# Performance work log

Hardware: AMD Instinct MI355X
Metric: run time of the kernel (lower is better)

## Reference

```python
import jax, jax.numpy as jnp
import numpy as np


def conv2d(x, w, groups=1, pad=0):
    # x: [N,C,H,W], w: [O, C//groups, kh, kw]
    return jax.lax.conv_general_dilated(
        x, w, window_strides=(1, 1), padding=[(pad, pad), (pad, pad)],
        dimension_numbers=("NCHW", "OIHW", "NCHW"), feature_group_count=groups)


def l2norm(x, eps=1e-12):
    # torch F.normalize over last dim: x / max(||x||_2, eps)
    n = jnp.sqrt(jnp.sum(x * x, axis=-1, keepdims=True))
    return x / jnp.maximum(n, eps)


def setup_inputs() -> dict:
    key = jax.random.key(0)
    dim, heads, b, H, W = 48, 8, 2, 256, 256
    ks = jax.random.split(key, 20)
    rn = lambda k, shp, s: (jax.random.normal(k, shp, dtype=jnp.float32) * s)
    return {
        "x1": rn(ks[0], (b, dim, H, W), 1.0),
        "x2": rn(ks[1], (b, dim, H, W), 1.0),
        "t1": jnp.ones((heads, 1, 1), jnp.float32),
        "t2": jnp.ones((heads, 1, 1), jnp.float32),
        "qkv1_w": rn(ks[2], (dim * 3, dim, 1, 1), 0.05),
        "qkv1_dw": rn(ks[3], (dim * 3, 1, 3, 3), 0.05),
        "qkv2_w": rn(ks[4], (dim * 3, dim, 1, 1), 0.05),
        "qkv2_dw": rn(ks[5], (dim * 3, 1, 3, 3), 0.05),
        "mid1_w": rn(ks[6], (dim, dim, 1, 1), 0.05),
        "mid2_w": rn(ks[7], (dim, dim, 1, 1), 0.05),
        "pE_w": rn(ks[8], (dim * 8, dim * 2, 1, 1), 0.05),
        "pE_dw": rn(ks[9], (dim * 8, 1, 3, 3), 0.05),
        "pE1_w": rn(ks[10], (dim * 4, dim, 1, 1), 0.05),
        "pE1_dw": rn(ks[11], (dim * 4, 1, 3, 3), 0.05),
        "pE2_w": rn(ks[12], (dim * 4, dim, 1, 1), 0.05),
        "pE2_dw": rn(ks[13], (dim * 4, 1, 3, 3), 0.05),
        "po1_w": rn(ks[14], (dim * 2, dim * 4, 1, 1), 0.05),
        "po2_w": rn(ks[15], (dim * 2, dim * 4, 1, 1), 0.05),
    }


def reference(x1, x2, t1, t2, qkv1_w, qkv1_dw, qkv2_w, qkv2_dw,
              mid1_w, mid2_w, pE_w, pE_dw, pE1_w, pE1_dw,
              pE2_w, pE2_dw, po1_w, po2_w):
    b, c, h, w = x1.shape
    heads = t1.shape[0]
    ch = c // heads  # channels per head

    def to_heads(t):  # [b, c, h, w] -> [b, heads, ch, h*w]
        return t.reshape(b, heads, ch, h * w)

    qkv1 = conv2d(conv2d(x1, qkv1_w), qkv1_dw, groups=3 * c, pad=1)
    q1, k1, v1 = jnp.split(qkv1, 3, axis=1)
    qkv2 = conv2d(conv2d(x2, qkv2_w), qkv2_dw, groups=3 * c, pad=1)
    q2, k2, v2 = jnp.split(qkv2, 3, axis=1)

    q1, k1, v1 = to_heads(q1), to_heads(k1), to_heads(v1)
    q2, k2, v2 = to_heads(q2), to_heads(k2), to_heads(v2)
    q1, k1 = l2norm(q1), l2norm(k1)
    q2, k2 = l2norm(q2), l2norm(k2)

    # channel cross-attention: [b, heads, ch, ch]
    attn1 = jnp.einsum("bhcn,bhdn->bhcd", q2, k1) * t1
    attn2 = jnp.einsum("bhcn,bhdn->bhcd", q1, k2) * t2
    out1 = jnp.einsum("bhcd,bhdn->bhcn", jax.nn.softmax(attn1, axis=-1), v1)
    out2 = jnp.einsum("bhcd,bhdn->bhcn", jax.nn.softmax(attn2, axis=-1), v2)
    out1 = out1.reshape(b, c, h, w)
    out2 = out2.reshape(b, c, h, w)

    x1 = x1 + conv2d(out1, mid1_w)
    x2 = x2 + conv2d(out2, mid2_w)
    out = jnp.concatenate([x1, x2], axis=1)  # [b, 2c, h, w]

    g = conv2d(conv2d(out, pE_w), pE_dw, groups=8 * c, pad=1)  # [b, 8c, h, w]
    g1, g2 = jnp.split(g, 2, axis=1)
    x1 = jax.nn.gelu(g1, approximate=False) * conv2d(conv2d(x1, pE1_w), pE1_dw, groups=4 * c, pad=1)
    x2 = jax.nn.gelu(g2, approximate=False) * conv2d(conv2d(x2, pE2_w), pE2_dw, groups=4 * c, pad=1)

    return out + conv2d(x1, po1_w) + conv2d(x2, po2_w)
```

## Files before the change

### kernel.cpp

```cpp
#include <hip/hip_runtime.h>
#include <math.h>

#define HW_ 65536

typedef __attribute__((ext_vector_type(8))) short b16x8;
typedef __attribute__((ext_vector_type(4))) short b16x4;
typedef __attribute__((ext_vector_type(4))) float f32x4;

__device__ __forceinline__ unsigned short f2b(float f) {
    union { float f; unsigned u; } v; v.f = f;
    unsigned r = v.u + 0x7fffu + ((v.u >> 16) & 1u);
    return (unsigned short)(r >> 16);
}
__device__ __forceinline__ float b2f(unsigned short h) {
    union { unsigned u; float f; } v; v.u = ((unsigned)h) << 16; return v.f;
}
__device__ __forceinline__ float gelu_f(float x) {
    float t = 0.7978845608f * fmaf(0.044715f * x, x * x, x);
    float e = __expf(2.f * t);
    float th = 1.f - 2.f / (e + 1.f);
    return 0.5f * x * (1.f + th);
}

__device__ __forceinline__ float wave_reduce_sum(float v) {
    #pragma unroll
    for (int off = 32; off; off >>= 1) v += __shfl_down(v, off, 64);
    return v;
}

__device__ __forceinline__ size_t baddr(long px, int CC, int g) {
    return (((size_t)(px >> 4)) * CC + g) * 128 + ((size_t)(px & 15) << 3);
}

__global__ __launch_bounds__(256) void wprep_k(
    const float* __restrict__ q1w, const float* __restrict__ q2w,
    const float* __restrict__ m1w, const float* __restrict__ m2w,
    const float* __restrict__ pEw, const float* __restrict__ p1w,
    const float* __restrict__ p2w, const float* __restrict__ o1w,
    const float* __restrict__ o2w,
    const float* __restrict__ q1dw, const float* __restrict__ q2dw,
    const float* __restrict__ pEdw, const float* __restrict__ p1dw,
    const float* __restrict__ p2dw,
    unsigned short* __restrict__ wt, float* __restrict__ dwt)
{
    const int idx = blockIdx.x * 256 + threadIdx.x;
    if (idx < 135168) {
        const int base[8] = {0,9216,18432,21504,24576,61440,98304,116736};
        int s = 0;
        #pragma unroll
        for (int i = 1; i < 8; i++) if (idx >= base[i]) s = i;
        const int local = idx - base[s];
        float v = 0.f;
        if (s < 4) {
            const int m = local >> 6, k = local & 63;
            const float* src = (s == 0) ? q1w : (s == 1) ? q2w : (s == 2) ? m1w : m2w;
            if (k < 48) v = src[m * 48 + k];
        } else if (s < 6) {
            const int br = s - 4;
            const int m = local / 96, k = local % 96;
            if (m < 192) {
                v = pEw[(size_t)(br * 192 + m) * 96 + k];
            } else {
                const float* p12 = br ? p2w : p1w;
                const int lo = br * 48, m2 = m - 192;
                if (k >= lo && k < lo + 48) v = p12[m2 * 48 + (k - lo)];
            }
        } else {
            const int m = local / 192, k = local % 192;
            v = ((s == 6) ? o1w : o2w)[m * 192 + k];
        }
        wt[idx] = f2b(v);
    } else if (idx < 135168 + 9504) {
        const int d = idx - 135168;
        const int dbase[5] = {0,1296,2592,6048,7776};
        const int Cs[5] = {144,144,384,192,192};
        int s = 0;
        #pragma unroll
        for (int i = 1; i < 5; i++) if (d >= dbase[i]) s = i;
        const int local = d - dbase[s], C = Cs[s];
        const int t = local / C, c = local % C;
        const float* src = (s == 0) ? q1dw : (s == 1) ? q2dw : (s == 2) ? pEdw
                         : (s == 3) ? p1dw : p2dw;
        dwt[d] = src[c * 9 + t];
    }
}

template<int BM, int KC, int NT, int BSRC, int EPI, bool GRIDSWAP>
__global__ __launch_bounds__(256) void gemm_k(
    const unsigned short* __restrict__ B16,
    const float* __restrict__ Bf32, int Cin,
    const unsigned short* __restrict__ W16,
    unsigned short* __restrict__ out16, int CCo, int Coff,
    float* __restrict__ outf, const unsigned short* __restrict__ res,
    const unsigned short* __restrict__ acc16)
{
    constexpr int MF = BM / 16;
    const int tid = threadIdx.x;
    const int lane = tid & 63, w = tid >> 6;
    const int lm = lane & 15, lk = lane >> 4;
    const int mb = GRIDSWAP ? blockIdx.x : blockIdx.y;
    const int pxblk = GRIDSWAP ? blockIdx.y : blockIdx.x;
    const int m0 = mb * BM;
    const long wavepx = ((long)pxblk * 4 + w) * (NT * 16);
    const long pxb0 = wavepx >> 4;

    f32x4 acc[NT][MF];
    #pragma unroll
    for (int nt = 0; nt < NT; nt++)
        #pragma unroll
        for (int m = 0; m < MF; m++)
            #pragma unroll
            for (int j = 0; j < 4; j++) acc[nt][m][j] = 0.f;

    #pragma unroll
    for (int kc = 0; kc < KC; kc++) {
        b16x8 a[MF];
        #pragma unroll
        for (int m = 0; m < MF; m++)
            a[m] = *(const b16x8*)&W16[(size_t)(m0 + m * 16 + lm) * (KC * 32) + kc * 32 + lk * 8];
        #pragma unroll
        for (int nt = 0; nt < NT; nt++) {
            b16x8 bb;
            if (BSRC == 0) {
                bb = *(const b16x8*)&B16[((pxb0 + nt) * (KC * 4) + (kc * 4 + lk)) * 128 + lm * 8];
            } else {
                const long px = wavepx + nt * 16 + lm;
                const int p = (int)(px & 65535), bat = (int)(px >> 16);
                #pragma unroll
                for (int j = 0; j < 8; j++) {
                    const int c = kc * 32 + lk * 8 + j;
                    float v = (c < Cin) ? Bf32[((size_t)(bat * Cin + c) << 16) + p] : 0.f;
                    bb[j] = (short)f2b(v);
                }
            }
            #pragma unroll
            for (int m = 0; m < MF; m++)
                acc[nt][m] = __builtin_amdgcn_mfma_f32_16x16x32_bf16(a[m], bb, acc[nt][m], 0, 0, 0);
        }
    }

    #pragma unroll
    for (int nt = 0; nt < NT; nt++) {
        const long px = wavepx + nt * 16 + lm;
        #pragma unroll
        for (int m = 0; m < MF; m++) {
            const int mrow = m * 16 + lk * 4;
            if (EPI == 0) {
                b16x4 o;
                #pragma unroll
                for (int j = 0; j < 4; j++) o[j] = (short)f2b(acc[nt][m][j]);
                const int ch = Coff + m0 + mrow;
                *(b16x4*)&out16[((pxb0 + nt) * CCo + (ch >> 3)) * 128 + lm * 8 + (ch & 7)] = o;
            } else if (EPI == 1) {
                const int p = (int)(px & 65535), bat = (int)(px >> 16);
                b16x4 r4 = *(const b16x4*)&res[((pxb0 + nt) * 12 + (mrow >> 3)) * 128 + lm * 8 + (mrow & 7)];
                #pragma unroll
                for (int j = 0; j < 4; j++)
                    outf[((size_t)(bat * 96 + mrow + j) << 16) + p]
                        = acc[nt][m][j] + b2f((unsigned short)r4[j]);
            } else if (EPI == 2) {
                const int p = (int)(px & 65535), bat = (int)(px >> 16);
                #pragma unroll
                for (int j = 0; j < 4; j++) {
                    const size_t adr = ((size_t)(bat * 96 + mrow + j) << 16) + p;
                    outf[adr] += acc[nt][m][j];
                }
            } else {
                const int p = (int)(px & 65535), bat = (int)(px >> 16);
                const size_t boffi = ((pxb0 + nt) * 12 + (mrow >> 3)) * 128 + lm * 8 + (mrow & 7);
                b16x4 r4 = *(const b16x4*)&res[boffi];
                b16x4 a4 = *(const b16x4*)&acc16[boffi];
                #pragma unroll
                for (int j = 0; j < 4; j++)
                    outf[((size_t)(bat * 96 + mrow + j) << 16) + p]
                        = acc[nt][m][j] + b2f((unsigned short)r4[j]) + b2f((unsigned short)a4[j]);
            }
        }
    }
}

__device__ __forceinline__ void unpack8(const uint4 u, float f[8]) {
    union { unsigned u; float f; } a;
    a.u = u.x << 16;         f[0] = a.f;
    a.u = u.x & 0xFFFF0000u; f[1] = a.f;
    a.u = u.y << 16;         f[2] = a.f;
    a.u = u.y & 0xFFFF0000u; f[3] = a.f;
    a.u = u.z << 16;         f[4] = a.f;
    a.u = u.z & 0xFFFF0000u; f[5] = a.f;
    a.u = u.w << 16;         f[6] = a.f;
    a.u = u.w & 0xFFFF0000u; f[7] = a.f;
}

__device__ __forceinline__ void dw_row4(
    float acc[4][8], const unsigned short* __restrict__ T,
    size_t cb, long lOff, long rOff, bool lval, bool rval,
    const float* __restrict__ wrow, int wstr)
{
    float w[3][8];
    #pragma unroll
    for (int tx = 0; tx < 3; tx++) {
        const float4 a = *(const float4*)(wrow + (size_t)tx * wstr);
        const float4 b = *(const float4*)(wrow + (size_t)tx * wstr + 4);
        w[tx][0] = a.x; w[tx][1] = a.y; w[tx][2] = a.z; w[tx][3] = a.w;
        w[tx][4] = b.x; w[tx][5] = b.y; w[tx][6] = b.z; w[tx][7] = b.w;
    }
    uint4 u[6];
    if (lval) u[0] = *(const uint4*)&T[cb + lOff];
    else      u[0] = make_uint4(0u, 0u, 0u, 0u);
    #pragma unroll
    for (int c = 0; c < 4; c++) u[c + 1] = *(const uint4*)&T[cb + (size_t)c * 8];
    if (rval) u[5] = *(const uint4*)&T[cb + rOff];
    else      u[5] = make_uint4(0u, 0u, 0u, 0u);

    #pragma unroll
    for (int d = 0; d < 6; d++) {
        float f[8];
        unpack8(u[d], f);
        #pragma unroll
        for (int tx = 0; tx < 3; tx++) {
            const int p = d - tx;
            if (p >= 0 && p < 4)
                #pragma unroll
                for (int j = 0; j < 8; j++)
                    acc[p][j] = fmaf(w[tx][j], f[j], acc[p][j]);
        }
    }
}

__global__ __launch_bounds__(256) void dw144_k(
    const unsigned short* __restrict__ in1, unsigned short* __restrict__ out1,
    const unsigned short* __restrict__ in2, unsigned short* __restrict__ out2,
    const float* __restrict__ dwt)
{
    const int z = blockIdx.z;
    const unsigned short* in = z ? in2 : in1;
    unsigned short* out = z ? out2 : out1;
    const float* wt = dwt + z * 1296;
    const int bx = blockIdx.x;
    const int sb = (bx & 7) * 288 + (bx >> 3);
    const int idx = sb * 256 + threadIdx.x;
    const int pbi = idx / 72;
    const int rem = idx - pbi * 72;
    const int g = rem >> 2, i = rem & 3;
    const long px0 = (long)pbi * 16 + i * 4;
    const int x0 = (int)(px0 & 255);
    const int y = (int)((px0 >> 8) & 255);
    const bool lval = x0 > 0, rval = x0 < 252;
    const int off = (int)(px0 & 15) * 8;
    const size_t cb0 = ((size_t)(px0 >> 4) * 18 + g) * 128 + off;
    const long lOff = (off == 0) ? (120 - 18 * 128) : -8;
    const long rOff = (off == 96) ? (18 * 128 - 96) : 32;
    const long dyStep = 16 * 18 * 128;

    float acc[4][8];
    #pragma unroll
    for (int p = 0; p < 4; p++)
        #pragma unroll
        for (int j = 0; j < 8; j++) acc[p][j] = 0.f;

    #pragma unroll
    for (int dy = -1; dy <= 1; dy++) {
        const int yy = y + dy;
        if ((unsigned)yy >= 256u) continue;
        const size_t cb = cb0 + (size_t)((long)dy * dyStep);
        dw_row4(acc, in, cb, lOff, rOff, lval, rval,
                wt + g * 8 + (size_t)(dy + 1) * 3 * 144, 144);
    }

    #pragma unroll
    for (int p = 0; p < 4; p++) {
        b16x8 o;
        #pragma unroll
        for (int j = 0; j < 8; j++) o[j] = (short)f2b(acc[p][j]);
        *(b16x8*)&out[cb0 + (size_t)p * 8] = o;
    }
}

__global__ __launch_bounds__(256) void dwtail_k(
    const unsigned short* __restrict__ GH, unsigned short* __restrict__ Xg,
    const float* __restrict__ dwtG, const float* __restrict__ dwtH)
{
    const int bx = blockIdx.x;
    const int sb = (bx & 7) * 384 + (bx >> 3);
    const int idx = sb * 256 + threadIdx.x;
    const int pbi = idx / 96;
    const int rem = idx - pbi * 96;
    const int g = rem >> 2, i = rem & 3;
    const long px0 = (long)pbi * 16 + i * 4;
    const int x0 = (int)(px0 & 255);
    const int y = (int)((px0 >> 8) & 255);
    const bool lval = x0 > 0, rval = x0 < 252;
    const int off = (int)(px0 & 15) * 8;
    const size_t cb0 = ((size_t)(px0 >> 4) * 48 + g) * 128 + off;
    const long lOff = (off == 0) ? (120 - 48 * 128) : -8;
    const long rOff = (off == 96) ? (48 * 128 - 96) : 32;
    const long dyStep = 16 * 48 * 128;

    float aG[4][8], aH[4][8];
    #pragma unroll
    for (int p = 0; p < 4; p++)
        #pragma unroll
        for (int j = 0; j < 8; j++) { aG[p][j] = 0.f; aH[p][j] = 0.f; }

    #pragma unroll
    for (int dy = -1; dy <= 1; dy++) {
        const int yy = y + dy;
        if ((unsigned)yy >= 256u) continue;
        const size_t cb = cb0 + (size_t)((long)dy * dyStep);
        dw_row4(aG, GH, cb, lOff, rOff, lval, rval,
                dwtG + g * 8 + (size_t)(dy + 1) * 3 * 384, 384);
        dw_row4(aH, GH, cb + 3072, lOff, rOff, lval, rval,
                dwtH + g * 8 + (size_t)(dy + 1) * 3 * 192, 192);
    }

    const size_t ob = ((size_t)(px0 >> 4) * 24 + g) * 128 + off;
    #pragma unroll
    for (int p = 0; p < 4; p++) {
        b16x8 o;
        #pragma unroll
        for (int j = 0; j < 8; j++)
            o[j] = (short)f2b(gelu_f(aG[p][j]) * aH[p][j]);
        *(b16x8*)&Xg[ob + (size_t)p * 8] = o;
    }
}

__global__ __launch_bounds__(256) void attnA_k(
    const unsigned short* __restrict__ Q1, const unsigned short* __restrict__ Q2,
    float* __restrict__ part)
{
    const int tid = threadIdx.x;
    const int chunk = blockIdx.x, bh = blockIdx.y, a = blockIdx.z;
    const int b = bh >> 3, h = bh & 7;
    const unsigned* Qq = (const unsigned*)(a ? Q1 : Q2);
    const unsigned* Qk = (const unsigned*)(a ? Q2 : Q1);
    const int u0 = h * 3;
    const int cq = u0 >> 2, o = u0 & 3;
    const int ck = (24 + u0) >> 2;

    float dot[36], nq[6], nk[6];
    #pragma unroll
    for (int i = 0; i < 36; i++) dot[i] = 0.f;
    #pragma unroll
    for (int i = 0; i < 6; i++) { nq[i] = 0.f; nk[i] = 0.f; }

    #pragma unroll 1
    for (int r = 0; r < 8; r++) {
        const long px = (long)b * 65536 + chunk * 2048 + r * 256 + tid;
        const size_t rowu = ((size_t)(px >> 4)) * 18 * 64 + ((px & 15) << 2);
        const uint4 qa = *(const uint4*)&Qq[rowu + (size_t)cq * 64];
        const uint4 qb = *(const uint4*)&Qq[rowu + (size_t)(cq + 1) * 64];
        const uint4 ka = *(const uint4*)&Qk[rowu + (size_t)ck * 64];
        const uint4 kb = *(const uint4*)&Qk[rowu + (size_t)(ck + 1) * 64];
        unsigned uq[3], uk[3];
        if (o == 0)      { uq[0]=qa.x; uq[1]=qa.y; uq[2]=qa.z; uk[0]=ka.x; uk[1]=ka.y; uk[2]=ka.z; }
        else if (o == 1) { uq[0]=qa.y; uq[1]=qa.z; uq[2]=qa.w; uk[0]=ka.y; uk[1]=ka.z; uk[2]=ka.w; }
        else if (o == 2) { uq[0]=qa.z; uq[1]=qa.w; uq[2]=qb.x; uk[0]=ka.z; uk[1]=ka.w; uk[2]=kb.x; }
        else             { uq[0]=qa.w; uq[1]=qb.x; uq[2]=qb.y; uk[0]=ka.w; uk[1]=kb.x; uk[2]=kb.y; }
        float q[6], k[6];
        #pragma unroll
        for (int i = 0; i < 3; i++) {
            union { unsigned u; float f; } lo, hi;
            lo.u = uq[i] << 16; hi.u = uq[i] & 0xFFFF0000u;
            q[2 * i] = lo.f; q[2 * i + 1] = hi.f;
            lo.u = uk[i] << 16; hi.u = uk[i] & 0xFFFF0000u;
            k[2 * i] = lo.f; k[2 * i + 1] = hi.f;
        }
        #pragma unroll
        for (int c = 0; c < 6; c++) nq[c] = fmaf(q[c], q[c], nq[c]);
        #pragma unroll
        for (int d = 0; d < 6; d++) nk[d] = fmaf(k[d], k[d], nk[d]);
        #pragma unroll
        for (int c = 0; c < 6; c++)
            #pragma unroll
            for (int d = 0; d < 6; d++) dot[c * 6 + d] = fmaf(q[c], k[d], dot[c * 6 + d]);
    }

    __shared__ float red[4][48];
    const int lane = tid & 63, wid = tid >> 6;
    #pragma unroll
    for (int i = 0; i < 48; i++) {
        float v = (i < 36) ? dot[i] : (i < 42 ? nq[i - 36] : nk[i - 42]);
        v = wave_reduce_sum(v);
        if (!lane) red[wid][i] = v;
    }
    __syncthreads();
    if (tid < 48)
        part[((size_t)((a * 16 + bh) * 32 + chunk)) * 48 + tid]
            = red[0][tid] + red[1][tid] + red[2][tid] + red[3][tid];
}

__global__ void attnB_k(const float* __restrict__ part,
                        const float* __restrict__ t1, const float* __restrict__ t2,
                        float* __restrict__ att)
{
    const int abh = blockIdx.x, tid = threadIdx.x;
    const int a = abh >> 4, b = (abh >> 3) & 1, h = abh & 7;
    __shared__ float s[48];
    if (tid < 48) {
        float v = 0.f;
        for (int ch = 0; ch < 32; ch++) v += part[((size_t)abh * 32 + ch) * 48 + tid];
        s[tid] = v;
    }
    __syncthreads();
    if (tid < 6) {
        const int c = tid;
        const float tv = a ? t2[h] : t1[h];
        const float qn = fmaxf(sqrtf(s[36 + c]), 1e-12f);
        float raw[6];
        #pragma unroll
        for (int d = 0; d < 6; d++)
            raw[d] = tv * s[c * 6 + d] / (qn * fmaxf(sqrtf(s[42 + d]), 1e-12f));
        float m = raw[0];
        #pragma unroll
        for (int d = 1; d < 6; d++) m = fmaxf(m, raw[d]);
        float e[6], sum = 0.f;
        #pragma unroll
        for (int d = 0; d < 6; d++) { e[d] = expf(raw[d] - m); sum += e[d]; }
        const float inv = 1.f / sum;
        #pragma unroll
        for (int d = 0; d < 6; d++)
            att[((size_t)(a * 2 + b) * 8 + h) * 36 + c * 6 + d] = e[d] * inv;
    }
}

__global__ __launch_bounds__(256) void mid_k(
    const unsigned short* __restrict__ Q1, const unsigned short* __restrict__ Q2,
    const float* __restrict__ att,
    const float* __restrict__ x1, const float* __restrict__ x2,
    const unsigned short* __restrict__ Wm, unsigned short* __restrict__ D16p)
{
    const int br = blockIdx.y;
    const unsigned short* Qv = br ? Q2 : Q1;
    const float* x = br ? x2 : x1;
    const unsigned short* W16 = Wm + br * 3072;
    const float* attb = att + br * 576;
    const int boff = br * 48;

    __shared__ float atts[288];
    __shared__ unsigned short S[256][72];
    const int tid = threadIdx.x;
    const long px = (long)blockIdx.x * 256 + tid;
    const int bat = (int)(px >> 16);

    for (int i = tid; i < 288; i += 256) atts[i] = attb[bat * 288 + i];

    float v[48];
    #pragma unroll
    for (int i = 0; i < 6; i++) {
        b16x8 t = *(const b16x8*)&Qv[baddr(px, 18, 12 + i)];
        #pragma unroll
        for (int j = 0; j < 8; j++) v[i * 8 + j] = b2f((unsigned short)t[j]);
    }
    __syncthreads();

    #pragma unroll
    for (int h = 0; h < 8; h++) {
        unsigned short sh[6];
        #pragma unroll
        for (int c = 0; c < 6; c++) {
            float s = 0.f;
            #pragma unroll
            for (int d = 0; d < 6; d++) s = fmaf(atts[h * 36 + c * 6 + d], v[h * 6 + d], s);
            sh[c] = f2b(s);
        }
        #pragma unroll
        for (int i = 0; i < 3; i++) {
            unsigned packed = (unsigned)sh[2 * i] | ((unsigned)sh[2 * i + 1] << 16);
            *(unsigned*)&S[tid][h * 6 + 2 * i] = packed;
        }
    }
    #pragma unroll
    for (int i = 0; i < 8; i++) *(unsigned*)&S[tid][48 + 2 * i] = 0u;
    __syncthreads();

    const int lane = tid & 63, w = tid >> 6;
    const int lm = lane & 15, lk = lane >> 4;
    f32x4 acc[4][3];
    #pragma unroll
    for (int nt = 0; nt < 4; nt++)
        #pragma unroll
        for (int m = 0; m < 3; m++)
            #pragma unroll
            for (int j = 0; j < 4; j++) acc[nt][m][j] = 0.f;

    #pragma unroll
    for (int kc = 0; kc < 2; kc++) {
        b16x8 a[3];
        #pragma unroll
        for (int m = 0; m < 3; m++)
            a[m] = *(const b16x8*)&W16[(size_t)(m * 16 + lm) * 64 + kc * 32 + lk * 8];
        #pragma unroll
        for (int nt = 0; nt < 4; nt++) {
            b16x8 bb = *(const b16x8*)&S[w * 64 + nt * 16 + lm][kc * 32 + lk * 8];
            #pragma unroll
            for (int m = 0; m < 3; m++)
                acc[nt][m] = __builtin_amdgcn_mfma_f32_16x16x32_bf16(a[m], bb, acc[nt][m], 0, 0, 0);
        }
    }

    #pragma unroll
    for (int nt = 0; nt < 4; nt++) {
        const long px2 = (long)blockIdx.x * 256 + w * 64 + nt * 16 + lm;
        const int p2 = (int)(px2 & 65535);
        const long pxb2 = px2 >> 4;
        #pragma unroll
        for (int m = 0; m < 3; m++) {
            const int row = m * 16 + lk * 4;
            b16x4 o;
            #pragma unroll
            for (int j = 0; j < 4; j++) {
                float xv = x[((size_t)(bat * 48 + row + j) << 16) + p2];
                o[j] = (short)f2b(acc[nt][m][j] + xv);
            }
            const int ch = boff + row;
            *(b16x4*)&D16p[(pxb2 * 12 + (ch >> 3)) * 128 + lm * 8 + (ch & 7)] = o;
        }
    }
}

extern "C" void kernel_launch(void* const* d_in, const int* in_sizes, int n_in,
                              void* d_out, int out_size, void* d_ws, size_t ws_size,
                              hipStream_t stream) {
    const float* x1      = (const float*)d_in[0];
    const float* x2      = (const float*)d_in[1];
    const float* t1      = (const float*)d_in[2];
    const float* t2      = (const float*)d_in[3];
    const float* qkv1_w  = (const float*)d_in[4];
    const float* qkv1_dw = (const float*)d_in[5];
    const float* qkv2_w  = (const float*)d_in[6];
    const float* qkv2_dw = (const float*)d_in[7];
    const float* mid1_w  = (const float*)d_in[8];
    const float* mid2_w  = (const float*)d_in[9];
    const float* pE_w    = (const float*)d_in[10];
    const float* pE_dw   = (const float*)d_in[11];
    const float* pE1_w   = (const float*)d_in[12];
    const float* pE1_dw  = (const float*)d_in[13];
    const float* pE2_w   = (const float*)d_in[14];
    const float* pE2_dw  = (const float*)d_in[15];
    const float* po1_w   = (const float*)d_in[16];
    const float* po2_w   = (const float*)d_in[17];
    float* dout = (float*)d_out;
    char* ws = (char*)d_ws;

    unsigned short* D16p  = (unsigned short*)(ws + 0);
    unsigned short* QKVc1 = (unsigned short*)(ws + 25165824);
    unsigned short* QKVc2 = (unsigned short*)(ws + 62914560);
    unsigned short* Q1    = (unsigned short*)(ws + 100663296);
    unsigned short* Q2    = (unsigned short*)(ws + 138412032);
    unsigned short* GH    = (unsigned short*)(ws + 25165824);
    unsigned short* Xg    = (unsigned short*)(ws + 125829120);
    float*          PART  = (float*)(ws + 176160768);
    float*          ATT   = (float*)(ws + 176357376);
    unsigned short* W16   = (unsigned short*)(ws + 176361984);
    float*          DWT   = (float*)(ws + 176632320);
    unsigned short* ACC   = (unsigned short*)(ws + 176670720);

    const dim3 blk(256);

    wprep_k<<<dim3(566), blk, 0, stream>>>(
        qkv1_w, qkv2_w, mid1_w, mid2_w, pE_w, pE1_w, pE2_w, po1_w, po2_w,
        qkv1_dw, qkv2_dw, pE_dw, pE1_dw, pE2_dw, W16, DWT);

    gemm_k<144,2,2,1,0,false><<<dim3(1024,1), blk, 0, stream>>>(
        nullptr, x1, 48, W16, QKVc1, 18, 0, nullptr, nullptr, nullptr);
    gemm_k<144,2,2,1,0,false><<<dim3(1024,1), blk, 0, stream>>>(
        nullptr, x2, 48, W16 + 9216, QKVc2, 18, 0, nullptr, nullptr, nullptr);
    dw144_k<<<dim3(2304,1,2), blk, 0, stream>>>(QKVc1, Q1, QKVc2, Q2, DWT);

    attnA_k<<<dim3(32,16,2), blk, 0, stream>>>(Q1, Q2, PART);
    attnB_k<<<dim3(32), dim3(64), 0, stream>>>(PART, t1, t2, ATT);

    mid_k<<<dim3(512,2), blk, 0, stream>>>(Q1, Q2, ATT, x1, x2, W16 + 18432, D16p);

    for (int br = 0; br < 2; br++) {
        gemm_k<96,3,2,0,0,true><<<dim3(4,1024), blk, 0, stream>>>(
            D16p, nullptr, 0, W16 + 24576 + br * 36864, GH, 48, 0,
            nullptr, nullptr, nullptr);
        dwtail_k<<<dim3(3072), blk, 0, stream>>>(
            GH, Xg, DWT + 2592 + br * 192, DWT + (br ? 7776 : 6048));
        if (br == 0)
            gemm_k<96,6,2,0,0,false><<<dim3(1024,1), blk, 0, stream>>>(
                Xg, nullptr, 0, W16 + 98304, ACC, 12, 0, nullptr, nullptr, nullptr);
        else
            gemm_k<96,6,2,0,3,false><<<dim3(1024,1), blk, 0, stream>>>(
                Xg, nullptr, 0, W16 + 116736, nullptr, 0, 0, dout, D16p, ACC);
    }
}
```

Baseline: 400.9 us.

## Fuse depthwise gelu-gate tail with po projection GEMM via shared memory

The depthwise 3x3 + GELU gating kernel and the following po 1x1 projection GEMM are merged into one kernel. Each 384-thread block computes a 64-pixel tile of the gated activations into LDS, then runs MFMA bf16 matmuls against the po weights and writes either the bf16 partial accumulator or the final fp32 output with residuals. This removes the global round trip of the Xg intermediate and one launch per branch. In exchange the block has lower parallelism for the GEMM, uses LDS per block, and reloads weights from global per block.

```diff
diff --git a/kernel.cpp b/kernel.cpp
--- a/kernel.cpp
+++ b/kernel.cpp
@@ -276,51 +276,105 @@
     }
 }
 
-__global__ __launch_bounds__(256) void dwtail_k(
-    const unsigned short* __restrict__ GH, unsigned short* __restrict__ Xg,
-    const float* __restrict__ dwtG, const float* __restrict__ dwtH)
-{
+template<int EPI>
+__global__ __launch_bounds__(384) void dwpo_k(
+    const unsigned short* __restrict__ GH,
+    const float* __restrict__ dwtG, const float* __restrict__ dwtH,
+    const unsigned short* __restrict__ Wpo,
+    unsigned short* __restrict__ ACC, float* __restrict__ dout,
+    const unsigned short* __restrict__ res,
+    const unsigned short* __restrict__ acc16)
+{
+    __shared__ unsigned short XgS[4 * 24 * 136];
     const int bx = blockIdx.x;
-    const int sb = (bx & 7) * 384 + (bx >> 3);
-    const int idx = sb * 256 + threadIdx.x;
-    const int pbi = idx / 96;
-    const int rem = idx - pbi * 96;
-    const int g = rem >> 2, i = rem & 3;
-    const long px0 = (long)pbi * 16 + i * 4;
-    const int x0 = (int)(px0 & 255);
-    const int y = (int)((px0 >> 8) & 255);
-    const bool lval = x0 > 0, rval = x0 < 252;
-    const int off = (int)(px0 & 15) * 8;
-    const size_t cb0 = ((size_t)(px0 >> 4) * 48 + g) * 128 + off;
-    const long lOff = (off == 0) ? (120 - 48 * 128) : -8;
-    const long rOff = (off == 96) ? (48 * 128 - 96) : 32;
-    const long dyStep = 16 * 48 * 128;
-
-    float aG[4][8], aH[4][8];
-    #pragma unroll
-    for (int p = 0; p < 4; p++)
-        #pragma unroll
-        for (int j = 0; j < 8; j++) { aG[p][j] = 0.f; aH[p][j] = 0.f; }
-
-    #pragma unroll
-    for (int dy = -1; dy <= 1; dy++) {
-        const int yy = y + dy;
-        if ((unsigned)yy >= 256u) continue;
-        const size_t cb = cb0 + (size_t)((long)dy * dyStep);
-        dw_row4(aG, GH, cb, lOff, rOff, lval, rval,
-                dwtG + g * 8 + (size_t)(dy + 1) * 3 * 384, 384);
-        dw_row4(aH, GH, cb + 3072, lOff, rOff, lval, rval,
-                dwtH + g * 8 + (size_t)(dy + 1) * 3 * 192, 192);
-    }
-
-    const size_t ob = ((size_t)(px0 >> 4) * 24 + g) * 128 + off;
-    #pragma unroll
-    for (int p = 0; p < 4; p++) {
-        b16x8 o;
-        #pragma unroll
-        for (int j = 0; j < 8; j++)
-            o[j] = (short)f2b(gelu_f(aG[p][j]) * aH[p][j]);
-        *(b16x8*)&Xg[ob + (size_t)p * 8] = o;
+    const int tile = (bx & 7) * 256 + (bx >> 3);
+    const int tid = threadIdx.x;
+
+    {
+        const int pg = tid / 24;
+        const int g  = tid - pg * 24;
+        const long px0 = (long)tile * 64 + pg * 4;
+        const int x0 = (int)(px0 & 255);
+        const int y = (int)((px0 >> 8) & 255);
+        const bool lval = x0 > 0, rval = x0 < 252;
+        const int off = (int)(px0 & 15) * 8;
+        const size_t cb0 = ((size_t)(px0 >> 4) * 48 + g) * 128 + off;
+        const long lOff = (off == 0) ? (120 - 48 * 128) : -8;
+        const long rOff = (off == 96) ? (48 * 128 - 96) : 32;
+        const long dyStep = 16 * 48 * 128;
+
+        float aG[4][8], aH[4][8];
+        #pragma unroll
+        for (int p = 0; p < 4; p++)
+            #pragma unroll
+            for (int j = 0; j < 8; j++) { aG[p][j] = 0.f; aH[p][j] = 0.f; }
+
+        #pragma unroll
+        for (int dy = -1; dy <= 1; dy++) {
+            const int yy = y + dy;
+            if ((unsigned)yy >= 256u) continue;
+            const size_t cb = cb0 + (size_t)((long)dy * dyStep);
+            dw_row4(aG, GH, cb, lOff, rOff, lval, rval,
+                    dwtG + g * 8 + (size_t)(dy + 1) * 3 * 384, 384);
+            dw_row4(aH, GH, cb + 3072, lOff, rOff, lval, rval,
+                    dwtH + g * 8 + (size_t)(dy + 1) * 3 * 192, 192);
+        }
+
+        const int pxl0 = pg * 4;
+        #pragma unroll
+        for (int p = 0; p < 4; p++) {
+            const int pxl = pxl0 + p;
+            b16x8 o;
+            #pragma unroll
+            for (int j = 0; j < 8; j++)
+                o[j] = (short)f2b(gelu_f(aG[p][j]) * aH[p][j]);
+            *(b16x8*)&XgS[((pxl >> 4) * 24 + g) * 136 + (pxl & 15) * 8] = o;
+        }
+    }
+    __syncthreads();
+
+    {
+        const int lane = tid & 63, w = tid >> 6;
+        const int lm = lane & 15, lk = lane >> 4;
+        const int m0 = w * 16;
+        f32x4 acc[4];
+        #pragma unroll
+        for (int nt = 0; nt < 4; nt++)
+            #pragma unroll
+            for (int j = 0; j < 4; j++) acc[nt][j] = 0.f;
+
+        #pragma unroll
+        for (int kc = 0; kc < 6; kc++) {
+            b16x8 a = *(const b16x8*)&Wpo[(size_t)(m0 + lm) * 192 + kc * 32 + lk * 8];
+            #pragma unroll
+            for (int nt = 0; nt < 4; nt++) {
+                b16x8 bb = *(const b16x8*)&XgS[(nt * 24 + kc * 4 + lk) * 136 + lm * 8];
+                acc[nt] = __builtin_amdgcn_mfma_f32_16x16x32_bf16(a, bb, acc[nt], 0, 0, 0);
+            }
+        }
+
+        const long pxb0 = (long)tile * 4;
+        const int ch = m0 + lk * 4;
+        #pragma unroll
+        for (int nt = 0; nt < 4; nt++) {
+            const long pxb = pxb0 + nt;
+            if (EPI == 0) {
+                b16x4 o;
+                #pragma unroll
+                for (int j = 0; j < 4; j++) o[j] = (short)f2b(acc[nt][j]);
+                *(b16x4*)&ACC[(pxb * 12 + (ch >> 3)) * 128 + lm * 8 + (ch & 7)] = o;
+            } else {
+                const long px = pxb * 16 + lm;
+                const int p = (int)(px & 65535), bat = (int)(px >> 16);
+                const size_t boffi = (pxb * 12 + (ch >> 3)) * 128 + lm * 8 + (ch & 7);
+                b16x4 r4 = *(const b16x4*)&res[boffi];
+                b16x4 a4 = *(const b16x4*)&acc16[boffi];
+                #pragma unroll
+                for (int j = 0; j < 4; j++)
+                    dout[((size_t)(bat * 96 + ch + j) << 16) + p]
+                        = acc[nt][j] + b2f((unsigned short)r4[j]) + b2f((unsigned short)a4[j]);
+            }
+        }
     }
 }
 
@@ -548,7 +602,6 @@
     unsigned short* Q1    = (unsigned short*)(ws + 100663296);
     unsigned short* Q2    = (unsigned short*)(ws + 138412032);
     unsigned short* GH    = (unsigned short*)(ws + 25165824);
-    unsigned short* Xg    = (unsigned short*)(ws + 125829120);
     float*          PART  = (float*)(ws + 176160768);
     float*          ATT   = (float*)(ws + 176357376);
     unsigned short* W16   = (unsigned short*)(ws + 176361984);
@@ -576,13 +629,13 @@
         gemm_k<96,3,2,0,0,true><<<dim3(4,1024), blk, 0, stream>>>(
             D16p, nullptr, 0, W16 + 24576 + br * 36864, GH, 48, 0,
             nullptr, nullptr, nullptr);
-        dwtail_k<<<dim3(3072), blk, 0, stream>>>(
-            GH, Xg, DWT + 2592 + br * 192, DWT + (br ? 7776 : 6048));
         if (br == 0)
-            gemm_k<96,6,2,0,0,false><<<dim3(1024,1), blk, 0, stream>>>(
-                Xg, nullptr, 0, W16 + 98304, ACC, 12, 0, nullptr, nullptr, nullptr);
+            dwpo_k<0><<<dim3(2048), dim3(384), 0, stream>>>(
+                GH, DWT + 2592, DWT + 6048, W16 + 98304,
+                ACC, nullptr, nullptr, nullptr);
         else
-            gemm_k<96,6,2,0,3,false><<<dim3(1024,1), blk, 0, stream>>>(
-                Xg, nullptr, 0, W16 + 116736, nullptr, 0, 0, dout, D16p, ACC);
-    }
-}
+            dwpo_k<3><<<dim3(2048), dim3(384), 0, stream>>>(
+                GH, DWT + 2592 + 192, DWT + 7776, W16 + 116736,
+                nullptr, dout, D16p, ACC);
+    }
+}
```

After: 407.4 us. No clear change (+1.6%).
